# Kernel tuning notes

Hardware: AMD Instinct MI355X
Metric: run time of the kernel (lower is better)

The kernel has to match this reference:

```python
import jax, jax.numpy as jnp
import numpy as np

N_HEADS = 16
D_EMBED = 1024
D_HEAD = D_EMBED // N_HEADS
CAUSAL = False


def setup_inputs() -> dict:
    key = jax.random.key(0)
    k1, k2, k3, k4, k5 = jax.random.split(key, 5)
    B, S, D = 4, 2048, D_EMBED
    scale = 1.0 / np.sqrt(D)
    return {
        "x": jax.random.normal(k1, (B, S, D), dtype=jnp.float32),
        "w_in": jax.random.normal(k2, (D, 3 * D), dtype=jnp.float32) * scale,
        "b_in": jax.random.normal(k3, (3 * D,), dtype=jnp.float32) * 0.02,
        "w_out": jax.random.normal(k4, (D, D), dtype=jnp.float32) * scale,
        "b_out": jax.random.normal(k5, (D,), dtype=jnp.float32) * 0.02,
    }


def reference(x, w_in, b_in, w_out, b_out):
    B, S, D = x.shape
    qkv = jnp.einsum("bsd,de->bse", x, w_in) + b_in  # [B,S,3D]
    q, k, v = jnp.split(qkv, 3, axis=-1)
    # split heads -> [B,H,S,Dh]
    def sh(t):
        return t.reshape(B, S, N_HEADS, D_HEAD).transpose(0, 2, 1, 3)
    q, k, v = sh(q), sh(k), sh(v)
    weight = jnp.einsum("bhsd,bhtd->bhst", q, k)  # [B,H,S,S]
    if CAUSAL:
        mask = jnp.triu(jnp.ones((S, S), dtype=bool), k=1)
        weight = jnp.where(mask, -jnp.inf, weight)
    weight = weight / np.sqrt(D_HEAD)
    weight = jax.nn.softmax(weight, axis=-1)
    out = jnp.einsum("bhst,bhtd->bhsd", weight, v)
    out = out.transpose(0, 2, 1, 3).reshape(B, S, D)
    return jnp.einsum("bsd,de->bse", out, w_out) + b_out
```

## Files before the change

### kernel.cpp

```cpp
#include <hip/hip_runtime.h>
#include <hip/hip_bf16.h>

typedef unsigned short u16;
typedef __attribute__((ext_vector_type(8))) short bf16x8;
typedef __attribute__((ext_vector_type(4))) float f32x4;

#define QSCALE 0.180336880f

#define DEV static __device__ __forceinline__

DEV u16 f2bf(float f) {
  union { float f; unsigned u; } v; v.f = f;
  unsigned r = v.u + 0x7fffu + ((v.u >> 16) & 1u);
  return (u16)(r >> 16);
}

DEV unsigned pk2(float a, float b) {
  union { __hip_bfloat162 h; unsigned u; } c;
  c.h = __float22bfloat162_rn(make_float2(a, b));
  return c.u;
}

DEV void gll16(void* lds, const void* g) {
  __builtin_amdgcn_global_load_lds(
      (const __attribute__((address_space(1))) unsigned int*)g,
      (__attribute__((address_space(3))) unsigned int*)lds, 16, 0, 0);
}

__global__ __launch_bounds__(256) void cvt_f32_to_bf16(const float* __restrict__ in,
                                                       u16* __restrict__ out, int n4) {
  int i = blockIdx.x * blockDim.x + threadIdx.x;
  int stride = gridDim.x * blockDim.x;
  for (; i < n4; i += stride) {
    float4 f = ((const float4*)in)[i];
    ushort4 u;
    u.x = f2bf(f.x); u.y = f2bf(f.y); u.z = f2bf(f.z); u.w = f2bf(f.w);
    ((ushort4*)out)[i] = u;
  }
}

__global__ __launch_bounds__(256) void transpose_cvt(const float* __restrict__ W,
                                                     u16* __restrict__ Wt,
                                                     int K, int N, int sn, float sval) {
  __shared__ u16 t[64][65];
  const int k0 = blockIdx.x * 64, n0 = blockIdx.y * 64;
  const int tid = threadIdx.x;
  const int rr = tid >> 4;
  const int cc = (tid & 15) * 4;
  const float scl = (n0 < sn) ? sval : 1.0f;
#pragma unroll
  for (int i = 0; i < 4; ++i) {
    const int row = rr * 4 + i;
    float4 f = *(const float4*)&W[(size_t)(k0 + row) * N + n0 + cc];
    t[row][cc + 0] = f2bf(f.x * scl);
    t[row][cc + 1] = f2bf(f.y * scl);
    t[row][cc + 2] = f2bf(f.z * scl);
    t[row][cc + 3] = f2bf(f.w * scl);
  }
  __syncthreads();
#pragma unroll
  for (int i = 0; i < 4; ++i) {
    const int n = rr * 4 + i;
    ushort4 u;
    u.x = t[cc + 0][n]; u.y = t[cc + 1][n]; u.z = t[cc + 2][n]; u.w = t[cc + 3][n];
    *(ushort4*)&Wt[(size_t)(n0 + n) * K + k0 + cc] = u;
  }
}

__global__ __launch_bounds__(256) void transpose_v(const u16* __restrict__ qkv,
                                                   u16* __restrict__ vT) {
  __shared__ u16 t[64][72];
  const int bh = blockIdx.y;
  const int b = bh >> 4, h = bh & 15;
  const int t0 = blockIdx.x * 64;
  const int tid = threadIdx.x;
  const int row = tid >> 2;
  const int cg = (tid & 3) * 16;
  const size_t src = (size_t)b * 2048 * 3072 + (size_t)(t0 + row) * 3072 + 2048 + h * 64 + cg;
  bf16x8 v0 = *(const bf16x8*)&qkv[src];
  bf16x8 v1 = *(const bf16x8*)&qkv[src + 8];
#pragma unroll
  for (int i = 0; i < 8; ++i) { t[row][cg + i] = (u16)v0[i]; t[row][cg + 8 + i] = (u16)v1[i]; }
  __syncthreads();
  const int d = tid >> 2;
  const int tg = (tid & 3) * 16;
  bf16x8 o0, o1;
#pragma unroll
  for (int i = 0; i < 8; ++i) { o0[i] = (short)t[tg + i][d]; o1[i] = (short)t[tg + 8 + i][d]; }
  u16* dst = &vT[((size_t)bh * 64 + d) * 2048 + t0 + tg];
  *(bf16x8*)dst = o0;
  *(bf16x8*)(dst + 8) = o1;
}

template<bool OUT_BF16>
__global__ __launch_bounds__(256) void gemm_bf16(const u16* __restrict__ A,
                                                 const u16* __restrict__ Bt,
                                                 const float* __restrict__ bias,
                                                 void* __restrict__ Cout,
                                                 int M, int N, int K, int qn,
                                                 u16* __restrict__ vTout, int vn0) {
  __shared__ __align__(16) u16 As[128][64];
  __shared__ __align__(16) u16 Bs[128][64];
  const int tid = threadIdx.x;
  const int wave = tid >> 6, lane = tid & 63;
  const int g = lane >> 4, lr = lane & 15;
  const int bm = blockIdx.x * 128, bn = blockIdx.y * 128;
  const int wm = (wave >> 1) * 64, wn = (wave & 1) * 64;
  f32x4 acc[4][4] = {};
  for (int kt = 0; kt < K; kt += 64) {
    __syncthreads();
#pragma unroll
    for (int j = 0; j < 4; ++j) {
      int chunk = wave * 4 + j;
      int e = chunk * 512 + lane * 8;
      int r = e >> 6, c = e & 63;
      gll16((u16*)As + chunk * 512, &A[(size_t)(bm + r) * K + kt + c]);
      gll16((u16*)Bs + chunk * 512, &Bt[(size_t)(bn + r) * K + kt + c]);
    }
    __syncthreads();
#pragma unroll
    for (int kk = 0; kk < 64; kk += 32) {
      bf16x8 af[4], bfr[4];
#pragma unroll
      for (int m = 0; m < 4; ++m)
        af[m] = *(const bf16x8*)&As[wm + m * 16 + lr][kk + g * 8];
#pragma unroll
      for (int n = 0; n < 4; ++n)
        bfr[n] = *(const bf16x8*)&Bs[wn + n * 16 + lr][kk + g * 8];
#pragma unroll
      for (int m = 0; m < 4; ++m)
#pragma unroll
        for (int n = 0; n < 4; ++n)
          acc[m][n] = __builtin_amdgcn_mfma_f32_16x16x32_bf16(af[m], bfr[n], acc[m][n], 0, 0, 0);
    }
  }
#pragma unroll
  for (int m = 0; m < 4; ++m) {
#pragma unroll
    for (int n = 0; n < 4; ++n) {
      const int col = bn + wn + n * 16 + lr;
      float bv = bias ? bias[col] : 0.f;
      if (col < qn) bv *= QSCALE;
      if (vTout != nullptr && col >= vn0) {
        const int hc = col - vn0;
#pragma unroll
        for (int r = 0; r < 4; ++r) {
          const int row = bm + wm + m * 16 + g * 4 + r;
          const size_t idx = (((size_t)(row >> 11) * 16 + (hc >> 6)) * 64 + (hc & 63)) * 2048
                             + (row & 2047);
          vTout[idx] = f2bf(acc[m][n][r] + bv);
        }
      } else {
#pragma unroll
        for (int r = 0; r < 4; ++r) {
          const int row = bm + wm + m * 16 + g * 4 + r;
          float v = acc[m][n][r] + bv;
          if (OUT_BF16) ((u16*)Cout)[(size_t)row * N + col] = f2bf(v);
          else          ((float*)Cout)[(size_t)row * N + col] = v;
        }
      }
    }
  }
}


DEV float rowmax2(const f32x4* s) {
  f32x4 t;
#pragma unroll
  for (int i = 0; i < 4; ++i) t[i] = fmaxf(s[0][i], s[1][i]);
  return fmaxf(fmaxf(t[0], t[1]), fmaxf(t[2], t[3]));
}

DEV void rescale(f32x4* o, float& lsum, float& m, float pm, int g) {
  float a = fmaxf(pm, __shfl_xor(pm, 16));
  a = fmaxf(a, __shfl_xor(a, 32));
  float mn = fmaxf(m, a);
  float sc = __builtin_amdgcn_exp2f(m - mn);
  float x0 = __shfl(sc, g * 4 + 0), x1 = __shfl(sc, g * 4 + 1);
  float x2 = __shfl(sc, g * 4 + 2), x3 = __shfl(sc, g * 4 + 3);
#pragma unroll
  for (int nd = 0; nd < 4; ++nd) {
    o[nd][0] *= x0; o[nd][1] *= x1; o[nd][2] *= x2; o[nd][3] *= x3;
  }
  lsum *= sc;
  m = mn;
}

DEV float expwrite2(const f32x4* s, float m, char* pbase, const int* pwo) {
  float su = 0.f;
#pragma unroll
  for (int n = 0; n < 2; ++n) {
    float p0 = __builtin_amdgcn_exp2f(s[n][0] - m);
    float p1 = __builtin_amdgcn_exp2f(s[n][1] - m);
    float p2 = __builtin_amdgcn_exp2f(s[n][2] - m);
    float p3 = __builtin_amdgcn_exp2f(s[n][3] - m);
    uint2 w;
    w.x = pk2(p0, p1);
    w.y = pk2(p2, p3);
    *(uint2*)(pbase + pwo[n]) = w;
    su += (p0 + p1) + (p2 + p3);
  }
  return su;
}

#define ATTN_BODY(BUF, PRE)                                                       \
  {                                                                               \
    if (PRE) {                                                                    \
      gll16((u16*)Ks[(BUF) ^ 1] + wave * 512, gk); gk += 32 * 3072;               \
      gll16((u16*)Vs[(BUF) ^ 1] + wave * 512, gv); gv += 32;                      \
    }                                                                             \
    const char* kb = (const char*)Ks[(BUF)];                                      \
    const char* vb = (const char*)Vs[(BUF)];                                      \
    f32x4 s0[2] = {}, s1[2] = {};                                                 \
    _Pragma("unroll")                                                             \
    for (int kk = 0; kk < 2; ++kk)                                                \
      _Pragma("unroll")                                                           \
      for (int n = 0; n < 2; ++n) {                                               \
        bf16x8 kf = *(const bf16x8*)(kb + koff[kk][n]);                           \
        s0[n] = __builtin_amdgcn_mfma_f32_16x16x32_bf16(kf, qf0[kk], s0[n], 0, 0, 0); \
        s1[n] = __builtin_amdgcn_mfma_f32_16x16x32_bf16(kf, qf1[kk], s1[n], 0, 0, 0); \
      }                                                                           \
    float pm0 = rowmax2(s0), pm1 = rowmax2(s1);                                   \
    if (!__all((pm0 <= m0 + 8.f) && (pm1 <= m1 + 8.f))) {                         \
      rescale(o0, lsum0, m0, pm0, g);                                             \
      rescale(o1, lsum1, m1, pm1, g);                                             \
    }                                                                             \
    lsum0 += expwrite2(s0, m0, pb, pwo);                                          \
    lsum1 += expwrite2(s1, m1, pb + 1024, pwo);                                   \
    bf16x8 pf0 = *(const bf16x8*)(pb + poff);                                     \
    bf16x8 pf1 = *(const bf16x8*)(pb + 1024 + poff);                              \
    _Pragma("unroll")                                                             \
    for (int nd = 0; nd < 4; ++nd) {                                              \
      bf16x8 vf = *(const bf16x8*)(vb + voff[nd]);                                \
      o0[nd] = __builtin_amdgcn_mfma_f32_16x16x32_bf16(pf0, vf, o0[nd], 0, 0, 0); \
      o1[nd] = __builtin_amdgcn_mfma_f32_16x16x32_bf16(pf1, vf, o1[nd], 0, 0, 0); \
    }                                                                             \
    __syncthreads();                                                              \
  }

__global__ __launch_bounds__(256, 4) void attn_kernel(const u16* __restrict__ qkv,
                                                      const u16* __restrict__ vT,
                                                      u16* __restrict__ out) {
  __shared__ __align__(16) u16 Ks[2][2048];
  __shared__ __align__(16) u16 Vs[2][2048];
  __shared__ __align__(16) u16 Ps[4][1024];
  const int tid = threadIdx.x;
  const int wave = tid >> 6, lane = tid & 63;
  const int g = lane >> 4, lr = lane & 15;
  const int bh = blockIdx.y;
  const int b = bh >> 4, h = bh & 15;
  const int q0 = blockIdx.x * 128;
  const size_t base = (size_t)b * 2048 * 3072;
  const u16* kg = qkv + base + 1024 + h * 64;
  const u16* vg = vT + (size_t)bh * 64 * 2048;

  const int qrow = q0 + wave * 32 + lr;
  bf16x8 qf0[2], qf1[2];
#pragma unroll
  for (int kk = 0; kk < 2; ++kk) {
    qf0[kk] = *(const bf16x8*)&qkv[base + (size_t)qrow * 3072 + h * 64 + kk * 32 + g * 8];
    qf1[kk] = *(const bf16x8*)&qkv[base + (size_t)(qrow + 16) * 3072 + h * 64 + kk * 32 + g * 8];
  }

  const int sw7 = (lr & 7) << 4;
  const int swv = ((lr ^ (lr >> 2)) & 3) << 4;
  int koff[2][2];
#pragma unroll
  for (int kk = 0; kk < 2; ++kk)
#pragma unroll
    for (int n = 0; n < 2; ++n)
      koff[kk][n] = (n * 16 + lr) * 128 + ((kk * 64 + g * 16) ^ sw7);
  int voff[4];
#pragma unroll
  for (int nd = 0; nd < 4; ++nd)
    voff[nd] = (nd * 16 + lr) * 64 + ((g * 16) ^ swv);
  const int poff = lr * 64 + ((g * 16) ^ swv);
  int pwo[2];
#pragma unroll
  for (int n = 0; n < 2; ++n)
    pwo[n] = lr * 64 + ((n * 32 + g * 8) ^ swv);
  char* const pb = (char*)Ps[wave];

  const int a = wave * 1024 + lane * 16;
  const int kr = a >> 7;
  const int kcb = (a & 127) ^ ((kr & 7) << 4);
  const int vr = a >> 6;
  const int vcb = (a & 63) ^ (((vr ^ (vr >> 2)) & 3) << 4);
  const u16* gk = kg + (size_t)kr * 3072 + (kcb >> 1);
  const u16* gv = vg + (size_t)vr * 2048 + (vcb >> 1);

  f32x4 o0[4] = {}, o1[4] = {};
  float m0 = -1e30f, m1 = -1e30f, lsum0 = 0.f, lsum1 = 0.f;

  gll16((u16*)Ks[0] + wave * 512, gk); gk += 32 * 3072;
  gll16((u16*)Vs[0] + wave * 512, gv); gv += 32;
  __syncthreads();

  for (int it2 = 0; it2 < 32; ++it2) {
    ATTN_BODY(0, 1)
    ATTN_BODY(1, it2 < 31)
  }

  float lf0 = lsum0 + __shfl_xor(lsum0, 16); lf0 += __shfl_xor(lf0, 32);
  float lf1 = lsum1 + __shfl_xor(lsum1, 16); lf1 += __shfl_xor(lf1, 32);
  float l00 = __shfl(lf0, g * 4 + 0), l01 = __shfl(lf0, g * 4 + 1);
  float l02 = __shfl(lf0, g * 4 + 2), l03 = __shfl(lf0, g * 4 + 3);
  float l10 = __shfl(lf1, g * 4 + 0), l11 = __shfl(lf1, g * 4 + 1);
  float l12 = __shfl(lf1, g * 4 + 2), l13 = __shfl(lf1, g * 4 + 3);
  const size_t orow0 = (size_t)b * 2048 + q0 + wave * 32;
#pragma unroll
  for (int nd = 0; nd < 4; ++nd) {
    const int dcol = h * 64 + nd * 16 + lr;
    out[(orow0 + g * 4 + 0) * 1024 + dcol] = f2bf(o0[nd][0] / l00);
    out[(orow0 + g * 4 + 1) * 1024 + dcol] = f2bf(o0[nd][1] / l01);
    out[(orow0 + g * 4 + 2) * 1024 + dcol] = f2bf(o0[nd][2] / l02);
    out[(orow0 + g * 4 + 3) * 1024 + dcol] = f2bf(o0[nd][3] / l03);
    out[(orow0 + 16 + g * 4 + 0) * 1024 + dcol] = f2bf(o1[nd][0] / l10);
    out[(orow0 + 16 + g * 4 + 1) * 1024 + dcol] = f2bf(o1[nd][1] / l11);
    out[(orow0 + 16 + g * 4 + 2) * 1024 + dcol] = f2bf(o1[nd][2] / l12);
    out[(orow0 + 16 + g * 4 + 3) * 1024 + dcol] = f2bf(o1[nd][3] / l13);
  }
}

extern "C" void kernel_launch(void* const* d_in, const int* in_sizes, int n_in,
                              void* d_out, int out_size, void* d_ws, size_t ws_size,
                              hipStream_t stream) {
  (void)in_sizes; (void)n_in; (void)out_size;
  const float* x     = (const float*)d_in[0];
  const float* w_in  = (const float*)d_in[1];
  const float* b_in  = (const float*)d_in[2];
  const float* w_out = (const float*)d_in[3];
  const float* b_out = (const float*)d_in[4];
  float* out = (float*)d_out;

  char* ws = (char*)d_ws;
  u16* Xbf   = (u16*)ws; ws += (size_t)8192 * 1024 * 2;
  u16* WinT  = (u16*)ws; ws += (size_t)3072 * 1024 * 2;
  u16* WoutT = (u16*)ws; ws += (size_t)1024 * 1024 * 2;
  u16* qkv   = (u16*)ws; ws += (size_t)8192 * 3072 * 2;
  u16* attno = (u16*)ws; ws += (size_t)8192 * 1024 * 2;
  u16* vTsep = (u16*)ws;

  const size_t fused_need = 92274688ull + 16777216ull;
  const bool fused = (ws_size >= fused_need);
  u16* vT = fused ? vTsep : Xbf;

  cvt_f32_to_bf16<<<2048, 256, 0, stream>>>(x, Xbf, 8192 * 1024 / 4);
  transpose_cvt<<<dim3(16, 48), 256, 0, stream>>>(w_in, WinT, 1024, 3072, 1024, QSCALE);
  transpose_cvt<<<dim3(16, 16), 256, 0, stream>>>(w_out, WoutT, 1024, 1024, 0, 1.0f);
  if (fused) {
    gemm_bf16<true ><<<dim3(64, 24), 256, 0, stream>>>(Xbf, WinT, b_in, qkv,
                                                       8192, 3072, 1024, 1024, vT, 2048);
  } else {
    gemm_bf16<true ><<<dim3(64, 24), 256, 0, stream>>>(Xbf, WinT, b_in, qkv,
                                                       8192, 3072, 1024, 1024, nullptr, 1 << 30);
    transpose_v<<<dim3(32, 64), 256, 0, stream>>>(qkv, vT);
  }
  attn_kernel<<<dim3(16, 64), 256, 0, stream>>>(qkv, vT, attno);
  gemm_bf16<false><<<dim3(64, 8), 256, 0, stream>>>(attno, WoutT, b_out, out,
                                                    8192, 1024, 1024, 0, nullptr, 1 << 30);
}
```

Before: 237.8 us.

## Switch attention to 32x32x16 MFMA with register-resident P via permlane32 swap

Rewrites the attention inner loop to use 32x32x16 bf16 MFMA tiles so S is computed with K as the A operand and Q as the B operand, leaving each lane with one query column. Softmax probabilities are packed to bf16 and rearranged in registers with v_permlane32_swap so they can feed the PV MFMA directly, removing the per-wave LDS staging buffer for P along with its writes, reads and address math. The K/V LDS swizzle and global-to-LDS mapping are redone to match, and s_setprio hints are placed around the MFMA sections. The risks are a higher register count for the 16-wide accumulators and correctness of the new layout mapping.

Result: no change. 239.8 us (+0.9%).

```diff
diff --git a/kernel.cpp b/kernel.cpp
--- a/kernel.cpp
+++ b/kernel.cpp
@@ -4,6 +4,7 @@
 typedef unsigned short u16;
 typedef __attribute__((ext_vector_type(8))) short bf16x8;
 typedef __attribute__((ext_vector_type(4))) float f32x4;
+typedef __attribute__((ext_vector_type(16))) float f32x16;
 
 #define QSCALE 0.180336880f
 
@@ -164,45 +165,6 @@
 }
 
 
-DEV float rowmax2(const f32x4* s) {
-  f32x4 t;
-#pragma unroll
-  for (int i = 0; i < 4; ++i) t[i] = fmaxf(s[0][i], s[1][i]);
-  return fmaxf(fmaxf(t[0], t[1]), fmaxf(t[2], t[3]));
-}
-
-DEV void rescale(f32x4* o, float& lsum, float& m, float pm, int g) {
-  float a = fmaxf(pm, __shfl_xor(pm, 16));
-  a = fmaxf(a, __shfl_xor(a, 32));
-  float mn = fmaxf(m, a);
-  float sc = __builtin_amdgcn_exp2f(m - mn);
-  float x0 = __shfl(sc, g * 4 + 0), x1 = __shfl(sc, g * 4 + 1);
-  float x2 = __shfl(sc, g * 4 + 2), x3 = __shfl(sc, g * 4 + 3);
-#pragma unroll
-  for (int nd = 0; nd < 4; ++nd) {
-    o[nd][0] *= x0; o[nd][1] *= x1; o[nd][2] *= x2; o[nd][3] *= x3;
-  }
-  lsum *= sc;
-  m = mn;
-}
-
-DEV float expwrite2(const f32x4* s, float m, char* pbase, const int* pwo) {
-  float su = 0.f;
-#pragma unroll
-  for (int n = 0; n < 2; ++n) {
-    float p0 = __builtin_amdgcn_exp2f(s[n][0] - m);
-    float p1 = __builtin_amdgcn_exp2f(s[n][1] - m);
-    float p2 = __builtin_amdgcn_exp2f(s[n][2] - m);
-    float p3 = __builtin_amdgcn_exp2f(s[n][3] - m);
-    uint2 w;
-    w.x = pk2(p0, p1);
-    w.y = pk2(p2, p3);
-    *(uint2*)(pbase + pwo[n]) = w;
-    su += (p0 + p1) + (p2 + p3);
-  }
-  return su;
-}
-
 #define ATTN_BODY(BUF, PRE)                                                       \
   {                                                                               \
     if (PRE) {                                                                    \
@@ -211,30 +173,61 @@
     }                                                                             \
     const char* kb = (const char*)Ks[(BUF)];                                      \
     const char* vb = (const char*)Vs[(BUF)];                                      \
-    f32x4 s0[2] = {}, s1[2] = {};                                                 \
+    f32x16 s = {};                                                                \
+    __builtin_amdgcn_s_setprio(1);                                                \
     _Pragma("unroll")                                                             \
-    for (int kk = 0; kk < 2; ++kk)                                                \
+    for (int kk = 0; kk < 4; ++kk) {                                              \
+      bf16x8 kf = *(const bf16x8*)(kb + koff[kk]);                                \
+      s = __builtin_amdgcn_mfma_f32_32x32x16_bf16(kf, qf[kk], s, 0, 0, 0);        \
+    }                                                                             \
+    __builtin_amdgcn_s_setprio(0);                                                \
+    float t0 = fmaxf(fmaxf(s[0], s[1]), fmaxf(s[2], s[3]));                       \
+    float t1 = fmaxf(fmaxf(s[4], s[5]), fmaxf(s[6], s[7]));                       \
+    float t2 = fmaxf(fmaxf(s[8], s[9]), fmaxf(s[10], s[11]));                     \
+    float t3 = fmaxf(fmaxf(s[12], s[13]), fmaxf(s[14], s[15]));                   \
+    float pmax = fmaxf(fmaxf(t0, t1), fmaxf(t2, t3));                             \
+    pmax = fmaxf(pmax, __shfl_xor(pmax, 32));                                     \
+    if (!__all(pmax <= m + 8.f)) {                                                \
+      float mn = fmaxf(m, pmax);                                                  \
+      float sc = __builtin_amdgcn_exp2f(m - mn);                                  \
       _Pragma("unroll")                                                           \
-      for (int n = 0; n < 2; ++n) {                                               \
-        bf16x8 kf = *(const bf16x8*)(kb + koff[kk][n]);                           \
-        s0[n] = __builtin_amdgcn_mfma_f32_16x16x32_bf16(kf, qf0[kk], s0[n], 0, 0, 0); \
-        s1[n] = __builtin_amdgcn_mfma_f32_16x16x32_bf16(kf, qf1[kk], s1[n], 0, 0, 0); \
+      for (int r = 0; r < 16; ++r) {                                              \
+        float scr = __shfl(sc, (r & 3) + 8 * (r >> 2) + 4 * hi);                  \
+        o0[r] *= scr; o1[r] *= scr;                                               \
       }                                                                           \
-    float pm0 = rowmax2(s0), pm1 = rowmax2(s1);                                   \
-    if (!__all((pm0 <= m0 + 8.f) && (pm1 <= m1 + 8.f))) {                         \
-      rescale(o0, lsum0, m0, pm0, g);                                             \
-      rescale(o1, lsum1, m1, pm1, g);                                             \
-    }                                                                             \
-    lsum0 += expwrite2(s0, m0, pb, pwo);                                          \
-    lsum1 += expwrite2(s1, m1, pb + 1024, pwo);                                   \
-    bf16x8 pf0 = *(const bf16x8*)(pb + poff);                                     \
-    bf16x8 pf1 = *(const bf16x8*)(pb + 1024 + poff);                              \
+      lsum *= sc;                                                                 \
+      m = mn;                                                                     \
+    }                                                                             \
+    float pr[16];                                                                 \
     _Pragma("unroll")                                                             \
-    for (int nd = 0; nd < 4; ++nd) {                                              \
-      bf16x8 vf = *(const bf16x8*)(vb + voff[nd]);                                \
-      o0[nd] = __builtin_amdgcn_mfma_f32_16x16x32_bf16(pf0, vf, o0[nd], 0, 0, 0); \
-      o1[nd] = __builtin_amdgcn_mfma_f32_16x16x32_bf16(pf1, vf, o1[nd], 0, 0, 0); \
-    }                                                                             \
+    for (int r = 0; r < 16; ++r) pr[r] = __builtin_amdgcn_exp2f(s[r] - m);        \
+    lsum += ((pr[0] + pr[1]) + (pr[2] + pr[3])) + ((pr[4] + pr[5]) + (pr[6] + pr[7])) \
+          + ((pr[8] + pr[9]) + (pr[10] + pr[11])) + ((pr[12] + pr[13]) + (pr[14] + pr[15])); \
+    union { unsigned u[4]; bf16x8 v; } pa0, pa1;                                  \
+    {                                                                             \
+      unsigned X0 = pk2(pr[0], pr[1]), X1 = pk2(pr[2], pr[3]);                    \
+      unsigned Y0 = pk2(pr[4], pr[5]), Y1 = pk2(pr[6], pr[7]);                    \
+      asm volatile("v_permlane32_swap_b32 %0, %1" : "+v"(X0), "+v"(Y0));          \
+      asm volatile("v_permlane32_swap_b32 %0, %1" : "+v"(X1), "+v"(Y1));          \
+      pa0.u[0] = X0; pa0.u[1] = X1; pa0.u[2] = Y0; pa0.u[3] = Y1;                 \
+      unsigned Z0 = pk2(pr[8], pr[9]), Z1 = pk2(pr[10], pr[11]);                  \
+      unsigned W0 = pk2(pr[12], pr[13]), W1 = pk2(pr[14], pr[15]);                \
+      asm volatile("v_permlane32_swap_b32 %0, %1" : "+v"(Z0), "+v"(W0));          \
+      asm volatile("v_permlane32_swap_b32 %0, %1" : "+v"(Z1), "+v"(W1));          \
+      pa1.u[0] = Z0; pa1.u[1] = Z1; pa1.u[2] = W0; pa1.u[3] = W1;                 \
+    }                                                                             \
+    __builtin_amdgcn_s_setprio(1);                                                \
+    {                                                                             \
+      bf16x8 vf00 = *(const bf16x8*)(vb + voff[0][0]);                            \
+      bf16x8 vf10 = *(const bf16x8*)(vb + voff[1][0]);                            \
+      o0 = __builtin_amdgcn_mfma_f32_32x32x16_bf16(pa0.v, vf00, o0, 0, 0, 0);     \
+      o1 = __builtin_amdgcn_mfma_f32_32x32x16_bf16(pa0.v, vf10, o1, 0, 0, 0);     \
+      bf16x8 vf01 = *(const bf16x8*)(vb + voff[0][1]);                            \
+      bf16x8 vf11 = *(const bf16x8*)(vb + voff[1][1]);                            \
+      o0 = __builtin_amdgcn_mfma_f32_32x32x16_bf16(pa1.v, vf01, o0, 0, 0, 0);     \
+      o1 = __builtin_amdgcn_mfma_f32_32x32x16_bf16(pa1.v, vf11, o1, 0, 0, 0);     \
+    }                                                                             \
+    __builtin_amdgcn_s_setprio(0);                                                \
     __syncthreads();                                                              \
   }
 
@@ -243,10 +236,9 @@
                                                       u16* __restrict__ out) {
   __shared__ __align__(16) u16 Ks[2][2048];
   __shared__ __align__(16) u16 Vs[2][2048];
-  __shared__ __align__(16) u16 Ps[4][1024];
   const int tid = threadIdx.x;
   const int wave = tid >> 6, lane = tid & 63;
-  const int g = lane >> 4, lr = lane & 15;
+  const int hi = lane >> 5, l31 = lane & 31;
   const int bh = blockIdx.y;
   const int b = bh >> 4, h = bh & 15;
   const int q0 = blockIdx.x * 128;
@@ -254,43 +246,33 @@
   const u16* kg = qkv + base + 1024 + h * 64;
   const u16* vg = vT + (size_t)bh * 64 * 2048;
 
-  const int qrow = q0 + wave * 32 + lr;
-  bf16x8 qf0[2], qf1[2];
-#pragma unroll
-  for (int kk = 0; kk < 2; ++kk) {
-    qf0[kk] = *(const bf16x8*)&qkv[base + (size_t)qrow * 3072 + h * 64 + kk * 32 + g * 8];
-    qf1[kk] = *(const bf16x8*)&qkv[base + (size_t)(qrow + 16) * 3072 + h * 64 + kk * 32 + g * 8];
-  }
-
-  const int sw7 = (lr & 7) << 4;
-  const int swv = ((lr ^ (lr >> 2)) & 3) << 4;
-  int koff[2][2];
-#pragma unroll
-  for (int kk = 0; kk < 2; ++kk)
-#pragma unroll
-    for (int n = 0; n < 2; ++n)
-      koff[kk][n] = (n * 16 + lr) * 128 + ((kk * 64 + g * 16) ^ sw7);
-  int voff[4];
-#pragma unroll
-  for (int nd = 0; nd < 4; ++nd)
-    voff[nd] = (nd * 16 + lr) * 64 + ((g * 16) ^ swv);
-  const int poff = lr * 64 + ((g * 16) ^ swv);
-  int pwo[2];
-#pragma unroll
-  for (int n = 0; n < 2; ++n)
-    pwo[n] = lr * 64 + ((n * 32 + g * 8) ^ swv);
-  char* const pb = (char*)Ps[wave];
-
-  const int a = wave * 1024 + lane * 16;
-  const int kr = a >> 7;
-  const int kcb = (a & 127) ^ ((kr & 7) << 4);
-  const int vr = a >> 6;
-  const int vcb = (a & 63) ^ (((vr ^ (vr >> 2)) & 3) << 4);
-  const u16* gk = kg + (size_t)kr * 3072 + (kcb >> 1);
-  const u16* gv = vg + (size_t)vr * 2048 + (vcb >> 1);
-
-  f32x4 o0[4] = {}, o1[4] = {};
-  float m0 = -1e30f, m1 = -1e30f, lsum0 = 0.f, lsum1 = 0.f;
+  const int qrow = q0 + wave * 32 + l31;
+  bf16x8 qf[4];
+#pragma unroll
+  for (int kk = 0; kk < 4; ++kk)
+    qf[kk] = *(const bf16x8*)&qkv[base + (size_t)qrow * 3072 + h * 64 + kk * 16 + hi * 8];
+
+  const int rsw = (l31 & 7) << 4;
+  int koff[4];
+#pragma unroll
+  for (int kk = 0; kk < 4; ++kk)
+    koff[kk] = l31 * 128 + ((kk * 32 + hi * 16) ^ rsw);
+  int voff[2][2];
+#pragma unroll
+  for (int dt = 0; dt < 2; ++dt)
+#pragma unroll
+    for (int kp = 0; kp < 2; ++kp)
+      voff[dt][kp] = l31 * 128 + ((dt * 64 + kp * 32 + hi * 16) ^ rsw);
+
+  const int a = tid * 16;
+  const int row = a >> 7;
+  const int cb = (a & 127) ^ ((row & 7) << 4);
+  const u16* gk = kg + (size_t)row * 3072 + (cb >> 1);
+  const int vd = row + (cb >> 6) * 32;
+  const u16* gv = vg + (size_t)vd * 2048 + ((cb & 63) >> 1);
+
+  f32x16 o0 = {}, o1 = {};
+  float m = -1e30f, lsum = 0.f;
 
   gll16((u16*)Ks[0] + wave * 512, gk); gk += 32 * 3072;
   gll16((u16*)Vs[0] + wave * 512, gv); gv += 32;
@@ -301,24 +283,15 @@
     ATTN_BODY(1, it2 < 31)
   }
 
-  float lf0 = lsum0 + __shfl_xor(lsum0, 16); lf0 += __shfl_xor(lf0, 32);
-  float lf1 = lsum1 + __shfl_xor(lsum1, 16); lf1 += __shfl_xor(lf1, 32);
-  float l00 = __shfl(lf0, g * 4 + 0), l01 = __shfl(lf0, g * 4 + 1);
-  float l02 = __shfl(lf0, g * 4 + 2), l03 = __shfl(lf0, g * 4 + 3);
-  float l10 = __shfl(lf1, g * 4 + 0), l11 = __shfl(lf1, g * 4 + 1);
-  float l12 = __shfl(lf1, g * 4 + 2), l13 = __shfl(lf1, g * 4 + 3);
+  float lt = lsum + __shfl_xor(lsum, 32);
   const size_t orow0 = (size_t)b * 2048 + q0 + wave * 32;
 #pragma unroll
-  for (int nd = 0; nd < 4; ++nd) {
-    const int dcol = h * 64 + nd * 16 + lr;
-    out[(orow0 + g * 4 + 0) * 1024 + dcol] = f2bf(o0[nd][0] / l00);
-    out[(orow0 + g * 4 + 1) * 1024 + dcol] = f2bf(o0[nd][1] / l01);
-    out[(orow0 + g * 4 + 2) * 1024 + dcol] = f2bf(o0[nd][2] / l02);
-    out[(orow0 + g * 4 + 3) * 1024 + dcol] = f2bf(o0[nd][3] / l03);
-    out[(orow0 + 16 + g * 4 + 0) * 1024 + dcol] = f2bf(o1[nd][0] / l10);
-    out[(orow0 + 16 + g * 4 + 1) * 1024 + dcol] = f2bf(o1[nd][1] / l11);
-    out[(orow0 + 16 + g * 4 + 2) * 1024 + dcol] = f2bf(o1[nd][2] / l12);
-    out[(orow0 + 16 + g * 4 + 3) * 1024 + dcol] = f2bf(o1[nd][3] / l13);
+  for (int r = 0; r < 16; ++r) {
+    const int crow = (r & 3) + 8 * (r >> 2) + 4 * hi;
+    const float li = __shfl(lt, crow);
+    u16* orow = out + (orow0 + crow) * 1024 + h * 64 + l31;
+    orow[0]  = f2bf(o0[r] / li);
+    orow[32] = f2bf(o1[r] / li);
   }
 }
 
```
